# Performance work log

Measured on AMD Instinct MI355X. Metric: run time of the kernel, lower is better.

Reference implementation:

```python
import jax, jax.numpy as jnp
import numpy as np

B, CIN, COUT, L = 8, 128, 128, 128
SCALE = 0.1


def _complex_mul(ar, ai, br, bi):
    return ar * br - ai * bi, ar * bi + ai * br


def _split_links(links):
    # links: (B, 4, L, L) -> (ux_r, ux_i, uy_r, uy_i) each (B, L, L)
    return links[:, 0], links[:, 1], links[:, 2], links[:, 3]


def _transport_forward(fr, fi, links, mu):
    ux_r, ux_i, uy_r, uy_i = _split_links(links)
    lr, li = (ux_r, ux_i) if mu == 0 else (uy_r, uy_i)
    # shift feature by -1 along spatial axis mu (axis mu+2 of (B,C,L,L))
    sr = jnp.roll(fr, shift=-1, axis=mu + 2)
    si = jnp.roll(fi, shift=-1, axis=mu + 2)
    return _complex_mul(lr[:, None], li[:, None], sr, si)


def _transport_backward(fr, fi, links, mu):
    ux_r, ux_i, uy_r, uy_i = _split_links(links)
    lr, li = (ux_r, ux_i) if mu == 0 else (uy_r, uy_i)
    cr, ci = lr, -li  # complex conjugate
    # roll conj link by +1 along its spatial axis mu (axis mu+1 of (B,L,L))
    cr = jnp.roll(cr, shift=1, axis=mu + 1)
    ci = jnp.roll(ci, shift=1, axis=mu + 1)
    sr = jnp.roll(fr, shift=1, axis=mu + 2)
    si = jnp.roll(fi, shift=1, axis=mu + 2)
    return _complex_mul(cr[:, None], ci[:, None], sr, si)


def setup_inputs() -> dict:
    key = jax.random.key(0)
    k1, k2, k3, k4, k5, k6 = jax.random.split(key, 6)
    feature_r = jax.random.normal(k1, (B, CIN, L, L), dtype=jnp.float32)
    feature_i = jax.random.normal(k2, (B, CIN, L, L), dtype=jnp.float32)
    links = jax.random.normal(k3, (B, 4, L, L), dtype=jnp.float32)
    center = SCALE * jax.random.normal(k4, (COUT, CIN), dtype=jnp.float32)
    forward_weight = SCALE * jax.random.normal(k5, (2, COUT, CIN), dtype=jnp.float32)
    backward_weight = SCALE * jax.random.normal(k6, (2, COUT, CIN), dtype=jnp.float32)
    return {
        "feature_r": feature_r,
        "feature_i": feature_i,
        "links": links,
        "center": center,
        "forward_weight": forward_weight,
        "backward_weight": backward_weight,
    }


def reference(feature_r, feature_i, links, center, forward_weight, backward_weight):
    mix = lambda w, x: jnp.einsum("oi,bixy->boxy", w, x)
    out_r = mix(center, feature_r)
    out_i = mix(center, feature_i)
    for mu in range(2):
        fwd_r, fwd_i = _transport_forward(feature_r, feature_i, links, mu)
        bwd_r, bwd_i = _transport_backward(feature_r, feature_i, links, mu)
        out_r = out_r + mix(forward_weight[mu], fwd_r) + mix(backward_weight[mu], bwd_r)
        out_i = out_i + mix(forward_weight[mu], fwd_i) + mix(backward_weight[mu], bwd_i)
    return out_r, out_i
```

## Files before the change

kernel.cpp:

```cpp
#include <hip/hip_runtime.h>
#include <stdint.h>


#define LL    128
#define NCIN  128
#define NCOUT 128
#define NB    8

typedef __attribute__((ext_vector_type(8)))  __bf16 bf16x8;
typedef __attribute__((ext_vector_type(4)))  __bf16 bf16x4;
typedef __attribute__((ext_vector_type(16))) float  f32x16;
typedef __attribute__((ext_vector_type(4)))  float  f32x4;
typedef __attribute__((ext_vector_type(4)))  uint32_t u32x4;

#define FP_BLOCK 132
#define FP_ROW   (32 * FP_BLOCK)
#define FP_DW    (3 * FP_ROW)
#define WROW     40
#define W_BYTES  (5 * 128 * WROW * 2)
#define LDS_BYTES (FP_DW * 4 + W_BYTES)

__device__ __forceinline__ float pair_lo_f32(uint32_t p) {
    uint32_t v = p << 16; return __builtin_bit_cast(float, v);
}
__device__ __forceinline__ float pair_hi_f32(uint32_t p) {
    uint32_t v = p & 0xFFFF0000u; return __builtin_bit_cast(float, v);
}

__global__ __launch_bounds__(512, 2)
void lconv_kernel(const float* __restrict__ frg, const float* __restrict__ fig,
                  const float* __restrict__ links, const float* __restrict__ wc,
                  const float* __restrict__ wf, const float* __restrict__ wb,
                  float* __restrict__ out)
{
    extern __shared__ char smem[];
    uint32_t* fp   = (uint32_t*)smem;
    __bf16*   wlds = (__bf16*)(smem + FP_DW * 4);

    const int tid  = threadIdx.x;
    const int lane = tid & 63;
    const int wv   = tid >> 6;
    const int l5   = lane >> 5;
    const int ln   = lane & 31;
    const int Mrow = wv >> 2;
    const int Ncol = wv & 3;

    const int bid     = blockIdx.x;
    const int logical = (bid & 7) * 128 + (bid >> 3);
    const int b = logical >> 7;
    const int x = logical & 127;
    const int xm = (x + 127) & 127;

    const int y  = Ncol * 32 + ln;
    const int yp = (y + 1) & 127;
    const int ym = (y + 127) & 127;

    const float* Lb = links + (size_t)b * 4 * LL * LL;
    const float lr1 =  Lb[(0*LL + x )*LL + y ];
    const float li1 =  Lb[(1*LL + x )*LL + y ];
    const float lr2 =  Lb[(0*LL + xm)*LL + y ];
    const float li2 = -Lb[(1*LL + xm)*LL + y ];
    const float lr3 =  Lb[(2*LL + x )*LL + y ];
    const float li3 =  Lb[(3*LL + x )*LL + y ];
    const float lr4 =  Lb[(2*LL + x )*LL + ym];
    const float li4 = -Lb[(3*LL + x )*LL + ym];

    f32x16 accR0 = {}, accR1 = {}, accI0 = {}, accI1 = {};

    for (int kc = 0; kc < 4; ++kc) {
        if (kc > 0) __syncthreads();

        #pragma unroll
        for (int j = 0; j < 6; ++j) {
            const int g   = tid + j * 512;
            const int row = g >> 10;
            const int rem = g & 1023;
            const int io  = rem >> 5;
            const int yb  = rem & 31;
            const int xs  = (x + row + 127) & 127;
            const size_t ga = (((size_t)(b * NCIN + kc * 32 + io)) * LL + xs) * LL
                            + (size_t)(yb * 4);
            const f32x4 fr4 = *(const f32x4*)(frg + ga);
            const f32x4 fi4 = *(const f32x4*)(fig + ga);
            u32x4 pk;
            #pragma unroll
            for (int v = 0; v < 4; ++v) {
                const uint32_t lo = (uint32_t)__builtin_bit_cast(uint16_t, (__bf16)fr4[v]);
                const uint32_t hi = (uint32_t)__builtin_bit_cast(uint16_t, (__bf16)fi4[v]);
                pk[v] = (hi << 16) | lo;
            }
            *(u32x4*)(fp + row * FP_ROW + yb * FP_BLOCK + io * 4) = pk;
        }

        #pragma unroll
        for (int j = 0; j < 10; ++j) {
            const int dd = j >> 1;
            const float* wsd = (dd == 0) ? wc
                             : (dd == 1) ? wf
                             : (dd == 2) ? wb
                             : (dd == 3) ? (wf + NCOUT * NCIN)
                                         : (wb + NCOUT * NCIN);
            const int r  = (j & 1) * 512 + tid;
            const int o  = r >> 3;
            const int k4 = (r & 7) * 4;
            const f32x4 w4 = *(const f32x4*)(wsd + o * NCIN + kc * 32 + k4);
            bf16x4 h;
            h[0] = (__bf16)w4.x; h[1] = (__bf16)w4.y;
            h[2] = (__bf16)w4.z; h[3] = (__bf16)w4.w;
            *(bf16x4*)&wlds[(dd * 128 + o) * WROW + k4] = h;
        }

        __syncthreads();

        #pragma unroll
        for (int d = 0; d < 5; ++d) {
            const int   row_d = (d == 1) ? 2 : (d == 2) ? 0 : 1;
            const int   ysrc  = (d == 3) ? yp : (d == 4) ? ym : y;
            const float lr    = (d == 1) ? lr1 : (d == 2) ? lr2 : (d == 3) ? lr3
                              : (d == 4) ? lr4 : 1.0f;
            const float li    = (d == 1) ? li1 : (d == 2) ? li2 : (d == 3) ? li3
                              : (d == 4) ? li4 : 0.0f;

            const int base = row_d * FP_ROW + (ysrc >> 2) * FP_BLOCK + (ysrc & 3);

            #pragma unroll
            for (int kk = 0; kk < 2; ++kk) {
                const int ib = kk * 16 + 8 * l5;
                uint32_t p[8];
                #pragma unroll
                for (int j = 0; j < 8; ++j)
                    p[j] = fp[base + (ib + j) * 4];

                bf16x8 Br, Bi;
                if (d == 0) {
                    u32x4 br, bi;
                    #pragma unroll
                    for (int q = 0; q < 4; ++q) {
                        br[q] = (p[2*q] & 0xFFFFu) | (p[2*q+1] << 16);
                        bi[q] = (p[2*q] >> 16)     | (p[2*q+1] & 0xFFFF0000u);
                    }
                    Br = __builtin_bit_cast(bf16x8, br);
                    Bi = __builtin_bit_cast(bf16x8, bi);
                } else {
                    #pragma unroll
                    for (int j = 0; j < 8; ++j) {
                        const float fr = pair_lo_f32(p[j]);
                        const float fi = pair_hi_f32(p[j]);
                        Br[j] = (__bf16)(lr * fr - li * fi);
                        Bi[j] = (__bf16)(lr * fi + li * fr);
                    }
                }

                #pragma unroll
                for (int mt = 0; mt < 2; ++mt) {
                    const int oo = (d * 128 + Mrow * 64 + mt * 32 + ln) * WROW
                                 + kk * 16 + 8 * l5;
                    const bf16x8 A = *(const bf16x8*)&wlds[oo];
                    f32x16& aR = mt ? accR1 : accR0;
                    f32x16& aI = mt ? accI1 : accI0;
                    aR = __builtin_amdgcn_mfma_f32_32x32x16_bf16(A, Br, aR, 0, 0, 0);
                    aI = __builtin_amdgcn_mfma_f32_32x32x16_bf16(A, Bi, aI, 0, 0, 0);
                }
            }
        }
    }

    const size_t OFF = (size_t)NB * NCOUT * LL * LL;
    #pragma unroll
    for (int mt = 0; mt < 2; ++mt) {
        const f32x16 aR = mt ? accR1 : accR0;
        const f32x16 aI = mt ? accI1 : accI0;
        const int ob = Mrow * 64 + mt * 32 + 4 * l5;
        #pragma unroll
        for (int r = 0; r < 16; ++r) {
            const int o = ob + (r & 3) + 8 * (r >> 2);
            const size_t idx = (((size_t)(b * NCOUT + o)) * LL + x) * LL + y;
            __builtin_nontemporal_store(aR[r], &out[idx]);
            __builtin_nontemporal_store(aI[r], &out[OFF + idx]);
        }
    }
}

extern "C" void kernel_launch(void* const* d_in, const int* in_sizes, int n_in,
                              void* d_out, int out_size, void* d_ws, size_t ws_size,
                              hipStream_t stream) {
    (void)in_sizes; (void)n_in; (void)out_size; (void)d_ws; (void)ws_size;
    const float* frg   = (const float*)d_in[0];
    const float* fig   = (const float*)d_in[1];
    const float* links = (const float*)d_in[2];
    const float* wc    = (const float*)d_in[3];
    const float* wf    = (const float*)d_in[4];
    const float* wb    = (const float*)d_in[5];
    float* out = (float*)d_out;

    hipFuncSetAttribute((const void*)lconv_kernel,
                        hipFuncAttributeMaxDynamicSharedMemorySize, LDS_BYTES);

    lconv_kernel<<<dim3(1024), dim3(512), LDS_BYTES, stream>>>(
        frg, fig, links, wc, wf, wb, out);
}
```

Measured before the change: 305.7 us.

## Halve input-channel chunk to shrink LDS and raise occupancy to four blocks

The K chunk per iteration drops from 32 to 16 input channels, which roughly halves the LDS footprint for the feature and weight tiles. Launch bounds rise from 2 to 4 blocks per CU so more waves can be resident. The cost is twice as many chunk iterations and barriers, and weight A fragments now come from two 8-byte LDS reads with a WROW of 20 instead of one 16-byte read. The dynamic-shared-memory attribute call is removed because the smaller allocation now fits under the default limit.

```diff
diff --git a/kernel.cpp b/kernel.cpp
--- a/kernel.cpp
+++ b/kernel.cpp
@@ -13,12 +13,12 @@
 typedef __attribute__((ext_vector_type(4)))  float  f32x4;
 typedef __attribute__((ext_vector_type(4)))  uint32_t u32x4;
 
-#define FP_BLOCK 132
-#define FP_ROW   (32 * FP_BLOCK)
-#define FP_DW    (3 * FP_ROW)
-#define WROW     40
-#define W_BYTES  (5 * 128 * WROW * 2)
-#define LDS_BYTES (FP_DW * 4 + W_BYTES)
+#define FPB   68
+#define FPROW (32 * FPB)
+#define FPDW  (3 * FPROW)
+#define WROW  20
+#define W_BYTES (5 * 128 * WROW * 2)
+#define LDS_BYTES (FPDW * 4 + W_BYTES)
 
 __device__ __forceinline__ float pair_lo_f32(uint32_t p) {
     uint32_t v = p << 16; return __builtin_bit_cast(float, v);
@@ -27,7 +27,7 @@
     uint32_t v = p & 0xFFFF0000u; return __builtin_bit_cast(float, v);
 }
 
-__global__ __launch_bounds__(512, 2)
+__global__ __launch_bounds__(512, 4)
 void lconv_kernel(const float* __restrict__ frg, const float* __restrict__ fig,
                   const float* __restrict__ links, const float* __restrict__ wc,
                   const float* __restrict__ wf, const float* __restrict__ wb,
@@ -35,7 +35,7 @@
 {
     extern __shared__ char smem[];
     uint32_t* fp   = (uint32_t*)smem;
-    __bf16*   wlds = (__bf16*)(smem + FP_DW * 4);
+    __bf16*   wlds = (__bf16*)(smem + FPDW * 4);
 
     const int tid  = threadIdx.x;
     const int lane = tid & 63;
@@ -67,18 +67,15 @@
 
     f32x16 accR0 = {}, accR1 = {}, accI0 = {}, accI1 = {};
 
-    for (int kc = 0; kc < 4; ++kc) {
+    for (int kc = 0; kc < 8; ++kc) {
         if (kc > 0) __syncthreads();
 
         #pragma unroll
-        for (int j = 0; j < 6; ++j) {
-            const int g   = tid + j * 512;
-            const int row = g >> 10;
-            const int rem = g & 1023;
-            const int io  = rem >> 5;
-            const int yb  = rem & 31;
-            const int xs  = (x + row + 127) & 127;
-            const size_t ga = (((size_t)(b * NCIN + kc * 32 + io)) * LL + xs) * LL
+        for (int j = 0; j < 3; ++j) {
+            const int io = tid >> 5;
+            const int yb = tid & 31;
+            const int xs = (x + j + 127) & 127;
+            const size_t ga = (((size_t)(b * NCIN + kc * 16 + io)) * LL + xs) * LL
                             + (size_t)(yb * 4);
             const f32x4 fr4 = *(const f32x4*)(frg + ga);
             const f32x4 fi4 = *(const f32x4*)(fig + ga);
@@ -89,25 +86,23 @@
                 const uint32_t hi = (uint32_t)__builtin_bit_cast(uint16_t, (__bf16)fi4[v]);
                 pk[v] = (hi << 16) | lo;
             }
-            *(u32x4*)(fp + row * FP_ROW + yb * FP_BLOCK + io * 4) = pk;
+            *(u32x4*)(fp + j * FPROW + yb * FPB + io * 4) = pk;
         }
 
         #pragma unroll
-        for (int j = 0; j < 10; ++j) {
-            const int dd = j >> 1;
-            const float* wsd = (dd == 0) ? wc
-                             : (dd == 1) ? wf
-                             : (dd == 2) ? wb
-                             : (dd == 3) ? (wf + NCOUT * NCIN)
-                                         : (wb + NCOUT * NCIN);
-            const int r  = (j & 1) * 512 + tid;
-            const int o  = r >> 3;
-            const int k4 = (r & 7) * 4;
-            const f32x4 w4 = *(const f32x4*)(wsd + o * NCIN + kc * 32 + k4);
+        for (int j = 0; j < 5; ++j) {
+            const float* wsd = (j == 0) ? wc
+                             : (j == 1) ? wf
+                             : (j == 2) ? wb
+                             : (j == 3) ? (wf + NCOUT * NCIN)
+                                        : (wb + NCOUT * NCIN);
+            const int o  = tid >> 2;
+            const int k4 = (tid & 3) * 4;
+            const f32x4 w4 = *(const f32x4*)(wsd + o * NCIN + kc * 16 + k4);
             bf16x4 h;
             h[0] = (__bf16)w4.x; h[1] = (__bf16)w4.y;
             h[2] = (__bf16)w4.z; h[3] = (__bf16)w4.w;
-            *(bf16x4*)&wlds[(dd * 128 + o) * WROW + k4] = h;
+            *(bf16x4*)&wlds[(j * 128 + o) * WROW + k4] = h;
         }
 
         __syncthreads();
@@ -121,46 +116,45 @@
             const float li    = (d == 1) ? li1 : (d == 2) ? li2 : (d == 3) ? li3
                               : (d == 4) ? li4 : 0.0f;
 
-            const int base = row_d * FP_ROW + (ysrc >> 2) * FP_BLOCK + (ysrc & 3);
+            const int base = row_d * FPROW + (ysrc >> 2) * FPB + (ysrc & 3);
+
+            uint32_t p[8];
+            #pragma unroll
+            for (int j = 0; j < 8; ++j)
+                p[j] = fp[base + (8 * l5 + j) * 4];
+
+            bf16x8 Br, Bi;
+            if (d == 0) {
+                u32x4 br, bi;
+                #pragma unroll
+                for (int q = 0; q < 4; ++q) {
+                    br[q] = (p[2*q] & 0xFFFFu) | (p[2*q+1] << 16);
+                    bi[q] = (p[2*q] >> 16)     | (p[2*q+1] & 0xFFFF0000u);
+                }
+                Br = __builtin_bit_cast(bf16x8, br);
+                Bi = __builtin_bit_cast(bf16x8, bi);
+            } else {
+                #pragma unroll
+                for (int j = 0; j < 8; ++j) {
+                    const float fr = pair_lo_f32(p[j]);
+                    const float fi = pair_hi_f32(p[j]);
+                    Br[j] = (__bf16)(lr * fr - li * fi);
+                    Bi[j] = (__bf16)(lr * fi + li * fr);
+                }
+            }
 
             #pragma unroll
-            for (int kk = 0; kk < 2; ++kk) {
-                const int ib = kk * 16 + 8 * l5;
-                uint32_t p[8];
+            for (int mt = 0; mt < 2; ++mt) {
+                const int ro = (d * 128 + Mrow * 64 + mt * 32 + ln) * WROW + 8 * l5;
+                const bf16x4 a0 = *(const bf16x4*)&wlds[ro];
+                const bf16x4 a1 = *(const bf16x4*)&wlds[ro + 4];
+                bf16x8 A;
                 #pragma unroll
-                for (int j = 0; j < 8; ++j)
-                    p[j] = fp[base + (ib + j) * 4];
-
-                bf16x8 Br, Bi;
-                if (d == 0) {
-                    u32x4 br, bi;
-                    #pragma unroll
-                    for (int q = 0; q < 4; ++q) {
-                        br[q] = (p[2*q] & 0xFFFFu) | (p[2*q+1] << 16);
-                        bi[q] = (p[2*q] >> 16)     | (p[2*q+1] & 0xFFFF0000u);
-                    }
-                    Br = __builtin_bit_cast(bf16x8, br);
-                    Bi = __builtin_bit_cast(bf16x8, bi);
-                } else {
-                    #pragma unroll
-                    for (int j = 0; j < 8; ++j) {
-                        const float fr = pair_lo_f32(p[j]);
-                        const float fi = pair_hi_f32(p[j]);
-                        Br[j] = (__bf16)(lr * fr - li * fi);
-                        Bi[j] = (__bf16)(lr * fi + li * fr);
-                    }
-                }
-
-                #pragma unroll
-                for (int mt = 0; mt < 2; ++mt) {
-                    const int oo = (d * 128 + Mrow * 64 + mt * 32 + ln) * WROW
-                                 + kk * 16 + 8 * l5;
-                    const bf16x8 A = *(const bf16x8*)&wlds[oo];
-                    f32x16& aR = mt ? accR1 : accR0;
-                    f32x16& aI = mt ? accI1 : accI0;
-                    aR = __builtin_amdgcn_mfma_f32_32x32x16_bf16(A, Br, aR, 0, 0, 0);
-                    aI = __builtin_amdgcn_mfma_f32_32x32x16_bf16(A, Bi, aI, 0, 0, 0);
-                }
+                for (int e = 0; e < 4; ++e) { A[e] = a0[e]; A[4 + e] = a1[e]; }
+                f32x16& aR = mt ? accR1 : accR0;
+                f32x16& aI = mt ? accI1 : accI0;
+                aR = __builtin_amdgcn_mfma_f32_32x32x16_bf16(A, Br, aR, 0, 0, 0);
+                aI = __builtin_amdgcn_mfma_f32_32x32x16_bf16(A, Bi, aI, 0, 0, 0);
             }
         }
     }
@@ -193,9 +187,6 @@
     const float* wb    = (const float*)d_in[5];
     float* out = (float*)d_out;
 
-    hipFuncSetAttribute((const void*)lconv_kernel,
-                        hipFuncAttributeMaxDynamicSharedMemorySize, LDS_BYTES);
-
     lconv_kernel<<<dim3(1024), dim3(512), LDS_BYTES, stream>>>(
         frg, fig, links, wc, wf, wb, out);
 }
```

Result: faster. 295.0 us (-3.5%).
